# Kernel tuning notes

Measured on AMD Instinct MI355X. Metric: run time of the kernel, lower is better.

Reference implementation:

```python
import jax, jax.numpy as jnp
import numpy as np

B, N, D, E, C, R = 4, 4096, 2048, 8, 2, 128
K = N * C // E  # tokens routed to each adapter (capacity) = 1024


def setup_inputs() -> dict:
    key = jax.random.key(0)
    ks = jax.random.split(key, 6)
    sc = lambda k, shape, s: (jax.random.normal(k, shape, jnp.float32) * s)
    return {
        "x": sc(ks[0], (B, N, D), 1.0),
        "residual": sc(ks[1], (B, N, D), 1.0),
        "Wg": sc(ks[2], (D, E), 1.0 / np.sqrt(D)),
        "bg": jnp.zeros((E,), jnp.float32),
        "Wd": sc(ks[3], (E, D, R), 1.0 / np.sqrt(D)),
        "bd": jnp.zeros((E, R), jnp.float32),
        "Wu": sc(ks[4], (E, R, D), 1.0 / np.sqrt(R)),
        "bu": jnp.zeros((E, D), jnp.float32),
    }


def reference(x, residual, Wg, bg, Wd, bd, Wu, bu):
    # Gate logits. NOTE: the original code's `nn.Softmax(X).dim` IS the raw
    # logits tensor, so top-k runs on UN-softmaxed logits (faithful quirk).
    logits = x @ Wg + bg                                   # [B,N,E]
    G, I = jax.lax.top_k(jnp.swapaxes(logits, 1, 2), K)    # [B,E,K] each

    # Dispatch: gather top-k tokens per adapter (== one-hot einsum in source).
    X_in = jnp.take_along_axis(x[:, None, :, :], I[..., None], axis=2)  # [B,E,K,D]

    # Per-adapter bottleneck MLP with residual (Adapter: up(relu(down(x))) + x).
    h = jax.nn.relu(jnp.einsum('bekd,edr->bekr', X_in, Wd) + bd[None, :, None, :])
    up = jnp.einsum('bekr,erd->bekd', h, Wu) + bu[None, :, None, :]
    X_e = up + X_in                                        # [B,E,K,D]

    # Weighted scatter-combine back to token positions (== one-hot einsum).
    contrib = (G[..., None] * X_e).reshape(B, E * K, D)
    idx = I.reshape(B, E * K)
    combine = jax.vmap(lambda i, v: jnp.zeros((N, D), x.dtype).at[i].add(v))(idx, contrib)
    return combine + residual
```

## Files before the change

### kernel.cpp

```cpp
#include <hip/hip_runtime.h>

#define B_ 4
#define N_ 4096
#define D_ 2048
#define E_ 8
#define R_ 128
#define K_ 1024

typedef __attribute__((ext_vector_type(8))) short bf16x8;
typedef __attribute__((ext_vector_type(4))) float f32x4;

__device__ inline unsigned short f2bf(float f) {
  unsigned u = __float_as_uint(f);
  unsigned r = (u + 0x7FFFu + ((u >> 16) & 1u)) >> 16;
  return (unsigned short)r;
}

__global__ __launch_bounds__(256) void gate_kernel(const float* __restrict__ x,
                                                   const float* __restrict__ Wg,
                                                   const float* __restrict__ bg,
                                                   float* __restrict__ logitsT) {
  int wave = threadIdx.x >> 6;
  int lane = threadIdx.x & 63;
  int token = blockIdx.x * 4 + wave;
  int b = token / N_;
  int n = token % N_;
  const float* xr = x + (size_t)token * D_;
  float acc[E_];
#pragma unroll
  for (int e = 0; e < E_; ++e) acc[e] = 0.f;
  for (int d = lane; d < D_; d += 64) {
    float xv = xr[d];
    const float* wr = Wg + d * E_;
#pragma unroll
    for (int e = 0; e < E_; ++e) acc[e] += xv * wr[e];
  }
#pragma unroll
  for (int off = 32; off > 0; off >>= 1) {
#pragma unroll
    for (int e = 0; e < E_; ++e) acc[e] += __shfl_down(acc[e], off, 64);
  }
  if (lane == 0) {
#pragma unroll
    for (int e = 0; e < E_; ++e)
      logitsT[((size_t)b * E_ + e) * N_ + n] = acc[e] + bg[e];
  }
}

__global__ __launch_bounds__(256) void topk_kernel(const float* __restrict__ logitsT,
                                                   int* __restrict__ I,
                                                   float* __restrict__ G) {
  __shared__ unsigned keys[N_];
  __shared__ float vals[N_];
  __shared__ int s_tie[N_];
  __shared__ unsigned s_cnt;
  int be = blockIdx.x;
  const float* lg = logitsT + (size_t)be * N_;
  int tid = threadIdx.x;
  for (int n = tid; n < N_; n += 256) {
    float v = lg[n];
    unsigned u = __float_as_uint(v);
    keys[n] = (u & 0x80000000u) ? ~u : (u | 0x80000000u);
    vals[n] = v;
  }
  __syncthreads();

  unsigned prefix = 0;
  int rem = K_;
  for (int bit = 31; bit >= 0; --bit) {
    if (tid == 0) s_cnt = 0;
    __syncthreads();
    unsigned hi_mask = (bit == 31) ? 0u : (0xFFFFFFFFu << (bit + 1));
    unsigned sel_mask = hi_mask | (1u << bit);
    unsigned want = prefix | (1u << bit);
    unsigned lc = 0;
    for (int n = tid; n < N_; n += 256)
      lc += ((keys[n] & sel_mask) == want) ? 1u : 0u;
    atomicAdd(&s_cnt, lc);
    __syncthreads();
    unsigned c = s_cnt;
    if ((int)c >= rem) prefix = want;
    else rem -= (int)c;
    __syncthreads();
  }
  unsigned kth = prefix;

  if (tid == 0) s_cnt = 0;
  __syncthreads();
  int* Ibe = I + (size_t)be * K_;
  float* Gbe = G + (size_t)be * K_;
  for (int n = tid; n < N_; n += 256) {
    if (keys[n] > kth) {
      unsigned p = atomicAdd(&s_cnt, 1u);
      Ibe[p] = n;
      Gbe[p] = vals[n];
    }
  }
  __syncthreads();
  if (tid == 0) s_cnt = 0;
  __syncthreads();
  for (int n = tid; n < N_; n += 256)
    if (keys[n] == kth) s_tie[atomicAdd(&s_cnt, 1u)] = n;
  __syncthreads();
  int t = (int)s_cnt;
  int base = K_ - rem;
  for (int i = tid; i < t; i += 256) {
    int n = s_tie[i];
    int rank = 0;
    for (int j = 0; j < t; ++j) rank += (s_tie[j] < n) ? 1 : 0;
    if (rank < rem) { Ibe[base + rank] = n; Gbe[base + rank] = vals[n]; }
  }
}

__global__ __launch_bounds__(256) void cvt_x_kernel(const float4* __restrict__ xin,
                                                    ushort4* __restrict__ xbf, int n4) {
  int i = blockIdx.x * 256 + threadIdx.x;
  if (i >= n4) return;
  float4 v = xin[i];
  ushort4 o;
  o.x = f2bf(v.x); o.y = f2bf(v.y); o.z = f2bf(v.z); o.w = f2bf(v.w);
  xbf[i] = o;
}

__global__ __launch_bounds__(256) void cvt_wd_kernel(const float* __restrict__ Wd,
                                                     unsigned short* __restrict__ WdT) {
  int t = blockIdx.x * 256 + threadIdx.x;
  int d = t & (D_ - 1);
  int r = (t >> 11) & (R_ - 1);
  int e = t >> 18;
  WdT[t] = f2bf(Wd[((size_t)e * D_ + d) * R_ + r]);
}

__global__ __launch_bounds__(256) void cvt_wu_kernel(const float* __restrict__ Wu,
                                                     unsigned short* __restrict__ WuT) {
  int t = blockIdx.x * 256 + threadIdx.x;
  int r = t & (R_ - 1);
  int d = (t >> 7) & (D_ - 1);
  int e = t >> 18;
  WuT[t] = f2bf(Wu[((size_t)e * R_ + r) * D_ + d]);
}

__global__ __launch_bounds__(256) void init_out_kernel(const float4* __restrict__ res,
                                                       float4* __restrict__ out, int n4) {
  int i = blockIdx.x * blockDim.x + threadIdx.x;
  if (i < n4) out[i] = res[i];
}

__global__ __launch_bounds__(256) void down_mfma(const unsigned short* __restrict__ xbf,
                                                 const unsigned short* __restrict__ WdT,
                                                 const float* __restrict__ bd,
                                                 const int* __restrict__ I,
                                                 unsigned short* __restrict__ h) {
  __shared__ unsigned short As[64 * 72] __attribute__((aligned(16)));
  __shared__ unsigned short Bs[128 * 72] __attribute__((aligned(16)));
  __shared__ int s_tok[64];
  int be = blockIdx.x;
  int m0 = blockIdx.y * 64;
  int b = be >> 3, e = be & 7;
  int tid = threadIdx.x;
  if (tid < 64) s_tok[tid] = I[be * K_ + m0 + tid];
  __syncthreads();
  int lane = tid & 63, wave = tid >> 6;
  int l15 = lane & 15, quad = lane >> 4;
  int wrow = (wave >> 1) * 32, wcol = (wave & 1) * 64;

  const unsigned short* srcA[2];
  int dstA[2];
#pragma unroll
  for (int i = 0; i < 2; ++i) {
    int g = tid + 256 * i;
    int row = g >> 3, part = g & 7;
    srcA[i] = xbf + ((size_t)(b * N_ + s_tok[row])) * D_ + part * 8;
    dstA[i] = row * 72 + part * 8;
  }
  const unsigned short* Wde = WdT + (size_t)e * R_ * D_;
  const unsigned short* srcB[4];
  int dstB[4];
#pragma unroll
  for (int i = 0; i < 4; ++i) {
    int g = tid + 256 * i;
    int row = g >> 3, part = g & 7;
    srcB[i] = Wde + (size_t)row * D_ + part * 8;
    dstB[i] = row * 72 + part * 8;
  }

  f32x4 zv = {0.f, 0.f, 0.f, 0.f};
  f32x4 acc[2][4];
#pragma unroll
  for (int mi = 0; mi < 2; ++mi)
#pragma unroll
    for (int ni = 0; ni < 4; ++ni) acc[mi][ni] = zv;

  for (int d0 = 0; d0 < D_; d0 += 64) {
#pragma unroll
    for (int i = 0; i < 2; ++i)
      *(uint4*)&As[dstA[i]] = *(const uint4*)(srcA[i] + d0);
#pragma unroll
    for (int i = 0; i < 4; ++i)
      *(uint4*)&Bs[dstB[i]] = *(const uint4*)(srcB[i] + d0);
    __syncthreads();
#pragma unroll
    for (int ks = 0; ks < 64; ks += 32) {
      bf16x8 a[2], bb[4];
#pragma unroll
      for (int mi = 0; mi < 2; ++mi)
        a[mi] = *(const bf16x8*)&As[(wrow + mi * 16 + l15) * 72 + ks + quad * 8];
#pragma unroll
      for (int ni = 0; ni < 4; ++ni)
        bb[ni] = *(const bf16x8*)&Bs[(wcol + ni * 16 + l15) * 72 + ks + quad * 8];
#pragma unroll
      for (int mi = 0; mi < 2; ++mi)
#pragma unroll
        for (int ni = 0; ni < 4; ++ni)
          acc[mi][ni] = __builtin_amdgcn_mfma_f32_16x16x32_bf16(a[mi], bb[ni], acc[mi][ni], 0, 0, 0);
    }
    __syncthreads();
  }
#pragma unroll
  for (int mi = 0; mi < 2; ++mi) {
#pragma unroll
    for (int ni = 0; ni < 4; ++ni) {
      int col = wcol + ni * 16 + l15;
      float bias = bd[e * R_ + col];
#pragma unroll
      for (int r = 0; r < 4; ++r) {
        int mrow = m0 + wrow + mi * 16 + quad * 4 + r;
        float v = acc[mi][ni][r] + bias;
        h[((size_t)be * K_ + mrow) * R_ + col] = f2bf(v > 0.f ? v : 0.f);
      }
    }
  }
}

__global__ __launch_bounds__(256) void up_mfma(const float* __restrict__ x,
                                               const unsigned short* __restrict__ WuT,
                                               const float* __restrict__ bu,
                                               const int* __restrict__ I,
                                               const float* __restrict__ G,
                                               const unsigned short* __restrict__ h,
                                               float* __restrict__ out, int e) {
  __shared__ unsigned short As[128 * 136] __attribute__((aligned(16)));
  __shared__ unsigned short Bs[128 * 136] __attribute__((aligned(16)));
  __shared__ int s_tok[128];
  __shared__ float s_g[128];
  int ntile = blockIdx.x;
  int mtile = blockIdx.y;
  int b = blockIdx.z;
  int be = b * E_ + e;
  int m0 = mtile * 128, n0 = ntile * 128;
  int tid = threadIdx.x;
  if (tid < 128) {
    s_tok[tid] = I[be * K_ + m0 + tid];
    s_g[tid] = G[be * K_ + m0 + tid];
  }
  const unsigned short* hbe = h + ((size_t)be * K_ + m0) * R_;
  const unsigned short* Wue = WuT + ((size_t)e * D_ + n0) * R_;
#pragma unroll
  for (int i = 0; i < 8; ++i) {
    int g = tid + 256 * i;
    int row = g >> 4, part = g & 15;
    *(uint4*)&As[row * 136 + part * 8] = *(const uint4*)(hbe + (size_t)row * R_ + part * 8);
  }
#pragma unroll
  for (int i = 0; i < 8; ++i) {
    int g = tid + 256 * i;
    int row = g >> 4, part = g & 15;
    *(uint4*)&Bs[row * 136 + part * 8] = *(const uint4*)(Wue + (size_t)row * R_ + part * 8);
  }
  __syncthreads();

  int lane = tid & 63, wave = tid >> 6;
  int l15 = lane & 15, quad = lane >> 4;
  int wrow = (wave >> 1) * 64, wcol = (wave & 1) * 64;
  f32x4 zv = {0.f, 0.f, 0.f, 0.f};
  f32x4 acc[4][4];
#pragma unroll
  for (int mi = 0; mi < 4; ++mi)
#pragma unroll
    for (int ni = 0; ni < 4; ++ni) acc[mi][ni] = zv;

#pragma unroll
  for (int ks = 0; ks < 128; ks += 32) {
    bf16x8 a[4], bb[4];
#pragma unroll
    for (int mi = 0; mi < 4; ++mi)
      a[mi] = *(const bf16x8*)&As[(wrow + mi * 16 + l15) * 136 + ks + quad * 8];
#pragma unroll
    for (int ni = 0; ni < 4; ++ni)
      bb[ni] = *(const bf16x8*)&Bs[(wcol + ni * 16 + l15) * 136 + ks + quad * 8];
#pragma unroll
    for (int mi = 0; mi < 4; ++mi)
#pragma unroll
      for (int ni = 0; ni < 4; ++ni)
        acc[mi][ni] = __builtin_amdgcn_mfma_f32_16x16x32_bf16(a[mi], bb[ni], acc[mi][ni], 0, 0, 0);
  }

#pragma unroll
  for (int mi = 0; mi < 4; ++mi) {
#pragma unroll
    for (int r = 0; r < 4; ++r) {
      int row = wrow + mi * 16 + quad * 4 + r;
      int tok = s_tok[row];
      float g = s_g[row];
      const float* xr = x + ((size_t)(b * N_ + tok)) * D_ + n0;
      float* outr = out + ((size_t)(b * N_ + tok)) * D_ + n0;
#pragma unroll
      for (int ni = 0; ni < 4; ++ni) {
        int col = wcol + ni * 16 + l15;
        float v = g * (acc[mi][ni][r] + bu[e * D_ + n0 + col] + xr[col]);
        outr[col] += v;
      }
    }
  }
}

extern "C" void kernel_launch(void* const* d_in, const int* in_sizes, int n_in,
                              void* d_out, int out_size, void* d_ws, size_t ws_size,
                              hipStream_t stream) {
  const float* x        = (const float*)d_in[0];
  const float* residual = (const float*)d_in[1];
  const float* Wg       = (const float*)d_in[2];
  const float* bg       = (const float*)d_in[3];
  const float* Wd       = (const float*)d_in[4];
  const float* bd       = (const float*)d_in[5];
  const float* Wu       = (const float*)d_in[6];
  const float* bu       = (const float*)d_in[7];
  float* out = (float*)d_out;

  char* p = (char*)d_ws;
  float* logitsT = (float*)p;            p += (size_t)B_ * E_ * N_ * 4;
  int* Ibuf = (int*)p;                   p += (size_t)B_ * E_ * K_ * 4;
  float* Gbuf = (float*)p;               p += (size_t)B_ * E_ * K_ * 4;
  unsigned short* xbf = (unsigned short*)p;  p += (size_t)B_ * N_ * D_ * 2;
  unsigned short* WdT = (unsigned short*)p;  p += (size_t)E_ * R_ * D_ * 2;
  unsigned short* WuT = (unsigned short*)p;  p += (size_t)E_ * D_ * R_ * 2;
  unsigned short* hbuf = (unsigned short*)p;

  gate_kernel<<<B_ * N_ / 4, 256, 0, stream>>>(x, Wg, bg, logitsT);
  topk_kernel<<<B_ * E_, 256, 0, stream>>>(logitsT, Ibuf, Gbuf);
  cvt_x_kernel<<<(B_ * N_ * D_ / 4 + 255) / 256, 256, 0, stream>>>(
      (const float4*)x, (ushort4*)xbf, B_ * N_ * D_ / 4);
  cvt_wd_kernel<<<E_ * D_ * R_ / 256, 256, 0, stream>>>(Wd, WdT);
  cvt_wu_kernel<<<E_ * D_ * R_ / 256, 256, 0, stream>>>(Wu, WuT);
  init_out_kernel<<<B_ * N_ * D_ / 4 / 256, 256, 0, stream>>>(
      (const float4*)residual, (float4*)out, B_ * N_ * D_ / 4);
  down_mfma<<<dim3(B_ * E_, K_ / 64), 256, 0, stream>>>(xbf, WdT, bd, Ibuf, hbuf);
  for (int e = 0; e < E_; ++e)
    up_mfma<<<dim3(D_ / 128, K_ / 128, B_), 256, 0, stream>>>(
        x, WuT, bu, Ibuf, Gbuf, hbuf, out, e);
}
```

Measured before the change: 729.6 us.

## Fuse x bf16 conversion into gate kernel and use radix-histogram top-k

The gate kernel now reads x as float4 and writes the bf16 copy in the same pass, which removes the separate conversion kernel and its extra 128MB read of x. The top-k kernel switches from a 32-pass bitwise radix select over all 4096 keys to a 4-pass 8-bit histogram select that narrows a candidate list each pass, and it runs with 1024 threads per block. Gate values are recovered from the order-preserving keys, so the vals array is dropped. The risks are shared-memory atomic contention on the histograms and the tie ranking done over the final candidate list.

```diff
diff --git a/kernel.cpp b/kernel.cpp
--- a/kernel.cpp
+++ b/kernel.cpp
@@ -19,21 +19,28 @@
 __global__ __launch_bounds__(256) void gate_kernel(const float* __restrict__ x,
                                                    const float* __restrict__ Wg,
                                                    const float* __restrict__ bg,
-                                                   float* __restrict__ logitsT) {
+                                                   float* __restrict__ logitsT,
+                                                   unsigned short* __restrict__ xbf) {
   int wave = threadIdx.x >> 6;
   int lane = threadIdx.x & 63;
   int token = blockIdx.x * 4 + wave;
-  int b = token / N_;
-  int n = token % N_;
+  int b = token >> 12;
+  int n = token & (N_ - 1);
   const float* xr = x + (size_t)token * D_;
+  unsigned short* xbr = xbf + (size_t)token * D_;
   float acc[E_];
 #pragma unroll
   for (int e = 0; e < E_; ++e) acc[e] = 0.f;
-  for (int d = lane; d < D_; d += 64) {
-    float xv = xr[d];
-    const float* wr = Wg + d * E_;
-#pragma unroll
-    for (int e = 0; e < E_; ++e) acc[e] += xv * wr[e];
+  for (int d0 = lane * 4; d0 < D_; d0 += 256) {
+    float4 xv = *(const float4*)(xr + d0);
+    ushort4 o;
+    o.x = f2bf(xv.x); o.y = f2bf(xv.y); o.z = f2bf(xv.z); o.w = f2bf(xv.w);
+    *(ushort4*)(xbr + d0) = o;
+    const float* wr = Wg + (size_t)d0 * E_;
+#pragma unroll
+    for (int e = 0; e < E_; ++e)
+      acc[e] += xv.x * wr[e] + xv.y * wr[E_ + e] + xv.z * wr[2 * E_ + e] +
+                xv.w * wr[3 * E_ + e];
   }
 #pragma unroll
   for (int off = 32; off > 0; off >>= 1) {
@@ -47,79 +54,118 @@
   }
 }
 
-__global__ __launch_bounds__(256) void topk_kernel(const float* __restrict__ logitsT,
-                                                   int* __restrict__ I,
-                                                   float* __restrict__ G) {
+__global__ __launch_bounds__(1024) void topk_kernel(const float* __restrict__ logitsT,
+                                                    int* __restrict__ I,
+                                                    float* __restrict__ G) {
   __shared__ unsigned keys[N_];
-  __shared__ float vals[N_];
-  __shared__ int s_tie[N_];
+  __shared__ unsigned hist[256];
+  __shared__ int candA[N_];
+  __shared__ int candB[N_];
   __shared__ unsigned s_cnt;
+  __shared__ unsigned s_prefix;
+  __shared__ int s_rem;
+
   int be = blockIdx.x;
   const float* lg = logitsT + (size_t)be * N_;
   int tid = threadIdx.x;
-  for (int n = tid; n < N_; n += 256) {
-    float v = lg[n];
-    unsigned u = __float_as_uint(v);
+
+  for (int n = tid; n < N_; n += 1024) {
+    unsigned u = __float_as_uint(lg[n]);
     keys[n] = (u & 0x80000000u) ? ~u : (u | 0x80000000u);
-    vals[n] = v;
-  }
-  __syncthreads();
-
-  unsigned prefix = 0;
-  int rem = K_;
-  for (int bit = 31; bit >= 0; --bit) {
+  }
+  if (tid < 256) hist[tid] = 0;
+  if (tid == 0) s_cnt = 0;
+  __syncthreads();
+
+  for (int n = tid; n < N_; n += 1024) atomicAdd(&hist[keys[n] >> 24], 1u);
+  __syncthreads();
+  if (tid == 0) {
+    int r = K_;
+    int d = 255;
+    for (; d > 0; --d) {
+      int c = (int)hist[d];
+      if (c >= r) break;
+      r -= c;
+    }
+    s_prefix = (unsigned)d << 24;
+    s_rem = r;
+  }
+  __syncthreads();
+  {
+    unsigned pfx = s_prefix;
+    for (int n = tid; n < N_; n += 1024)
+      if ((keys[n] & 0xFF000000u) == pfx) candA[atomicAdd(&s_cnt, 1u)] = n;
+  }
+  __syncthreads();
+  int nc = (int)s_cnt;
+
+  int* cur = candA;
+  int* nxt = candB;
+#pragma unroll
+  for (int pass = 1; pass < 4; ++pass) {
+    int shift = 24 - 8 * pass;
+    __syncthreads();
+    if (tid < 256) hist[tid] = 0;
     if (tid == 0) s_cnt = 0;
     __syncthreads();
-    unsigned hi_mask = (bit == 31) ? 0u : (0xFFFFFFFFu << (bit + 1));
-    unsigned sel_mask = hi_mask | (1u << bit);
-    unsigned want = prefix | (1u << bit);
-    unsigned lc = 0;
-    for (int n = tid; n < N_; n += 256)
-      lc += ((keys[n] & sel_mask) == want) ? 1u : 0u;
-    atomicAdd(&s_cnt, lc);
-    __syncthreads();
-    unsigned c = s_cnt;
-    if ((int)c >= rem) prefix = want;
-    else rem -= (int)c;
-    __syncthreads();
-  }
-  unsigned kth = prefix;
-
+    for (int i = tid; i < nc; i += 1024)
+      atomicAdd(&hist[(keys[cur[i]] >> shift) & 255u], 1u);
+    __syncthreads();
+    if (tid == 0) {
+      int r = s_rem;
+      int d = 255;
+      for (; d > 0; --d) {
+        int c = (int)hist[d];
+        if (c >= r) break;
+        r -= c;
+      }
+      s_prefix |= (unsigned)d << shift;
+      s_rem = r;
+    }
+    __syncthreads();
+    {
+      unsigned want = s_prefix;
+      unsigned msk = 0xFFFFFFFFu << shift;
+      for (int i = tid; i < nc; i += 1024) {
+        int n = cur[i];
+        if ((keys[n] & msk) == want) nxt[atomicAdd(&s_cnt, 1u)] = n;
+      }
+    }
+    __syncthreads();
+    nc = (int)s_cnt;
+    int* t = cur; cur = nxt; nxt = t;
+  }
+
+  unsigned kth = s_prefix;
+  int rem = s_rem;
+  int nties = nc;
+  __syncthreads();
   if (tid == 0) s_cnt = 0;
   __syncthreads();
+
   int* Ibe = I + (size_t)be * K_;
   float* Gbe = G + (size_t)be * K_;
-  for (int n = tid; n < N_; n += 256) {
-    if (keys[n] > kth) {
+  for (int n = tid; n < N_; n += 1024) {
+    unsigned k = keys[n];
+    if (k > kth) {
       unsigned p = atomicAdd(&s_cnt, 1u);
+      unsigned u = (k & 0x80000000u) ? (k ^ 0x80000000u) : ~k;
       Ibe[p] = n;
-      Gbe[p] = vals[n];
-    }
-  }
-  __syncthreads();
-  if (tid == 0) s_cnt = 0;
-  __syncthreads();
-  for (int n = tid; n < N_; n += 256)
-    if (keys[n] == kth) s_tie[atomicAdd(&s_cnt, 1u)] = n;
-  __syncthreads();
-  int t = (int)s_cnt;
+      Gbe[p] = __uint_as_float(u);
+    }
+  }
   int base = K_ - rem;
-  for (int i = tid; i < t; i += 256) {
-    int n = s_tie[i];
+  unsigned uk = (kth & 0x80000000u) ? (kth ^ 0x80000000u) : ~kth;
+  float tieval = __uint_as_float(uk);
+  for (int i = tid; i < nties; i += 1024) {
+    int n = cur[i];
     int rank = 0;
-    for (int j = 0; j < t; ++j) rank += (s_tie[j] < n) ? 1 : 0;
-    if (rank < rem) { Ibe[base + rank] = n; Gbe[base + rank] = vals[n]; }
-  }
-}
-
-__global__ __launch_bounds__(256) void cvt_x_kernel(const float4* __restrict__ xin,
-                                                    ushort4* __restrict__ xbf, int n4) {
-  int i = blockIdx.x * 256 + threadIdx.x;
-  if (i >= n4) return;
-  float4 v = xin[i];
-  ushort4 o;
-  o.x = f2bf(v.x); o.y = f2bf(v.y); o.z = f2bf(v.z); o.w = f2bf(v.w);
-  xbf[i] = o;
+    for (int j = 0; j < nties; ++j) rank += (cur[j] < n) ? 1 : 0;
+    if (rank < rem) {
+      Ibe[base + rank] = n;
+      Gbe[base + rank] = tieval;
+    }
+  }
 }
 
 __global__ __launch_bounds__(256) void cvt_wd_kernel(const float* __restrict__ Wd,
@@ -336,10 +382,8 @@
   unsigned short* WuT = (unsigned short*)p;  p += (size_t)E_ * D_ * R_ * 2;
   unsigned short* hbuf = (unsigned short*)p;
 
-  gate_kernel<<<B_ * N_ / 4, 256, 0, stream>>>(x, Wg, bg, logitsT);
-  topk_kernel<<<B_ * E_, 256, 0, stream>>>(logitsT, Ibuf, Gbuf);
-  cvt_x_kernel<<<(B_ * N_ * D_ / 4 + 255) / 256, 256, 0, stream>>>(
-      (const float4*)x, (ushort4*)xbf, B_ * N_ * D_ / 4);
+  gate_kernel<<<B_ * N_ / 4, 256, 0, stream>>>(x, Wg, bg, logitsT, xbf);
+  topk_kernel<<<B_ * E_, 1024, 0, stream>>>(logitsT, Ibuf, Gbuf);
   cvt_wd_kernel<<<E_ * D_ * R_ / 256, 256, 0, stream>>>(Wd, WdT);
   cvt_wu_kernel<<<E_ * D_ * R_ / 256, 256, 0, stream>>>(Wu, WuT);
   init_out_kernel<<<B_ * N_ * D_ / 4 / 256, 256, 0, stream>>>(
```

New measurement: 713.6 us. -2.2%, faster.
